# Performance work log

Hardware: AMD Instinct MI355X
Metric: run time of the kernel (lower is better)

## Reference

```python
import jax, jax.numpy as jnp
import numpy as np

INPUT_SIZE = 256
OUTPUT_SIZE = 128
N = 8192
SLOPE = 0.01
NEG_BIG = -9e15


def setup_inputs() -> dict:
    key = jax.random.key(0)
    k_h, k_adj, k_W, k_a = jax.random.split(key, 4)
    h = jax.random.normal(k_h, (N, INPUT_SIZE), dtype=jnp.float32)
    adj = jax.random.randint(k_adj, (N, N), 0, 2, dtype=jnp.int32)
    # xavier_uniform with gain=1.414
    gain = 1.414
    lim_W = gain * np.sqrt(6.0 / (INPUT_SIZE + OUTPUT_SIZE))
    W = jax.random.uniform(k_W, (INPUT_SIZE, OUTPUT_SIZE), dtype=jnp.float32, minval=-lim_W, maxval=lim_W)
    lim_a = gain * np.sqrt(6.0 / (2 * OUTPUT_SIZE + 1))
    a = jax.random.uniform(k_a, (2 * OUTPUT_SIZE, 1), dtype=jnp.float32, minval=-lim_a, maxval=lim_a)
    return {"h": h, "adj": adj, "W": W, "a": a}


def reference(h, adj, W, a):
    # Wh: [N, F]
    Wh = h @ W
    Fo = Wh.shape[1]
    # Original builds [N, N, 2F] concat then matmul with a; equivalent to
    # e[i, j] = leaky_relu(Wh[i] . a[:F] + Wh[j] . a[F:]) via broadcasting.
    src = Wh @ a[:Fo, 0]   # [N]
    dst = Wh @ a[Fo:, 0]   # [N]
    e = jax.nn.leaky_relu(src[:, None] + dst[None, :], negative_slope=SLOPE)  # [N, N]
    att = jnp.where(adj > 0, e, NEG_BIG)
    att = jax.nn.softmax(att, axis=1)
    return att @ Wh
```

## Files before the change

kernel.cpp:

```cpp
#include <hip/hip_runtime.h>
#include <hip/hip_bf16.h>

typedef unsigned short u16;
typedef unsigned char u8;
typedef unsigned int u32;
typedef __attribute__((ext_vector_type(8))) short short8;
typedef __attribute__((ext_vector_type(4))) float f32x4;

#define NN 8192
#define KIN 256
#define FOUT 128
#define KW 2048
#define L2E 1.4426950408889634f

__device__ __forceinline__ float exp2fast(float x) { return __builtin_amdgcn_exp2f(x); }

__device__ __forceinline__ u16 f2bf(float f) {
    u32 u = __float_as_uint(f);
    u32 r = ((u >> 16) & 1u) + 0x7fffu;
    return (u16)((u + r) >> 16);
}
__device__ __forceinline__ u32 pk_bf16(float a, float b) {
    union { __hip_bfloat162 h2; u32 u; } cv;
    cv.h2 = __float22bfloat162_rn(make_float2(a, b));
    return cv.u;
}
__device__ __forceinline__ u32 fkey(float f) {
    u32 b = __float_as_uint(f);
    return (b & 0x80000000u) ? ~b : (b | 0x80000000u);
}
__device__ __forceinline__ float funkey(u32 k) {
    u32 b = (k & 0x80000000u) ? (k & 0x7fffffffu) : ~k;
    return __uint_as_float(b);
}

__global__ __launch_bounds__(256) void k1_wh(
    const float* __restrict__ h, const float* __restrict__ W, const float* __restrict__ a,
    u16* __restrict__ whfrag,
    float* __restrict__ src, float* __restrict__ dl2e, u32* __restrict__ gmaxk)
{
    __shared__ float hT[64][36];
    __shared__ u16   lt[128][40];
    __shared__ float sd[32][2];
    const int t  = threadIdx.x;
    const int m0 = blockIdx.x * 32;
    const int rq = t >> 5, cq = t & 31;

    float acc[4][4];
#pragma unroll
    for (int i = 0; i < 4; i++)
#pragma unroll
        for (int j = 0; j < 4; j++) acc[i][j] = 0.f;
    if (t < 64) sd[t >> 1][t & 1] = 0.f;

    for (int kt = 0; kt < KIN; kt += 64) {
        __syncthreads();
#pragma unroll
        for (int s2 = 0; s2 < 2; s2++) {
            int f = s2 * 256 + t;
            int r = f >> 4, kc = (f & 15) * 4;
            float4 hv = *(const float4*)(h + (size_t)(m0 + r) * KIN + kt + kc);
            hT[kc + 0][r] = hv.x; hT[kc + 1][r] = hv.y;
            hT[kc + 2][r] = hv.z; hT[kc + 3][r] = hv.w;
        }
        __syncthreads();
        for (int k = 0; k < 64; k++) {
            float4 wv = *(const float4*)(W + (size_t)(kt + k) * FOUT + cq * 4);
            float h0 = hT[k][rq * 4 + 0], h1 = hT[k][rq * 4 + 1];
            float h2 = hT[k][rq * 4 + 2], h3 = hT[k][rq * 4 + 3];
            acc[0][0] += h0 * wv.x; acc[0][1] += h0 * wv.y; acc[0][2] += h0 * wv.z; acc[0][3] += h0 * wv.w;
            acc[1][0] += h1 * wv.x; acc[1][1] += h1 * wv.y; acc[1][2] += h1 * wv.z; acc[1][3] += h1 * wv.w;
            acc[2][0] += h2 * wv.x; acc[2][1] += h2 * wv.y; acc[2][2] += h2 * wv.z; acc[2][3] += h2 * wv.w;
            acc[3][0] += h3 * wv.x; acc[3][1] += h3 * wv.y; acc[3][2] += h3 * wv.z; acc[3][3] += h3 * wv.w;
        }
    }
#pragma unroll
    for (int i = 0; i < 4; i++) {
        float sp = 0.f, dp = 0.f;
#pragma unroll
        for (int j = 0; j < 4; j++) {
            sp += acc[i][j] * a[cq * 4 + j];
            dp += acc[i][j] * a[FOUT + cq * 4 + j];
            lt[cq * 4 + j][rq * 4 + i] = f2bf(acc[i][j]);
        }
        atomicAdd(&sd[rq * 4 + i][0], sp);
        atomicAdd(&sd[rq * 4 + i][1], dp);
    }
    __syncthreads();
    if (t < 32) { src[m0 + t] = sd[t][0]; dl2e[m0 + t] = sd[t][1] * L2E; }
    if (t < 64) {
        float v = (t < 32) ? sd[t][1] : -3.0e38f;
#pragma unroll
        for (int off = 32; off >= 1; off >>= 1) v = fmaxf(v, __shfl_down(v, off));
        if (t == 0) atomicMax(gmaxk, fkey(v));
    }
    const int kstep = blockIdx.x;
#pragma unroll
    for (int p = 0; p < 2; p++) {
        int f = p * 256 + t;
        int nt = f >> 6;
        int l  = f & 63;
        short8 v = *(const short8*)&lt[nt * 16 + (l & 15)][(l >> 4) * 8];
        *(short8*)(whfrag + ((size_t)(kstep * 8 + nt) * 64 + l) * 8) = v;
    }
}

__global__ __launch_bounds__(256, 4) void k2_attn(
    const int* __restrict__ adj, const float* __restrict__ src, const float* __restrict__ dl2e,
    const u16* __restrict__ whfrag, const u32* __restrict__ gmaxk,
    float* __restrict__ out)
{
    __shared__ u8  mask[4][16][512];
    __shared__ u16 Pall[4][16][40];
    const int t = threadIdx.x;
    const int lane = t & 63, wave = t >> 6;
    const int i0 = blockIdx.x * 16;
    const int l15 = lane & 15, quad = lane >> 4;
    const int r0 = lane >> 3, r1 = 8 + r0;
    const int co = (lane & 7) * 4;
    const int cbase = wave * KW;

#pragma unroll
    for (int r = 0; r < 16; r++) {
        const int* ap = adj + (size_t)(i0 + r) * NN + cbase;
#pragma unroll
        for (int c = 0; c < 8; c++) {
            int4 v = *(const int4*)(ap + c * 256 + lane * 4);
            mask[wave][r][c * 64 + lane] =
                (u8)((v.x > 0) | ((v.y > 0) << 1) | ((v.z > 0) << 2) | ((v.w > 0) << 3));
        }
    }

    const float gm = funkey(*gmaxk) * L2E;
    float s0 = src[i0 + r0] * L2E, s1 = src[i0 + r1] * L2E;
    float xm0 = s0 + gm, xm1 = s1 + gm;
    float C0 = fmaxf(xm0, 0.01f * xm0), C1 = fmaxf(xm1, 0.01f * xm1);
    const float y10 = s0 - C0, y20 = 0.01f * s0 - C0;
    const float y11 = s1 - C1, y21 = 0.01f * s1 - C1;

    u16 (*P)[40] = Pall[wave];
    f32x4 acc[8];
#pragma unroll
    for (int nt = 0; nt < 8; nt++) acc[nt] = {0.f, 0.f, 0.f, 0.f};
    float ps0 = 0.f, ps1 = 0.f;

    for (int kk = 0; kk < 64; ++kk) {
        const int kb = cbase + kk * 32;

        uint4 bv[8];
        const u16* wf = whfrag + ((size_t)((kb >> 5) * 8) * 64 + lane) * 8;
#pragma unroll
        for (int nt = 0; nt < 8; nt++)
            bv[nt] = *(const uint4*)(wf + (size_t)nt * 64 * 8);

        u32 n0 = mask[wave][r0][kk * 8 + (lane & 7)];
        u32 n1 = mask[wave][r1][kk * 8 + (lane & 7)];
        float4 d = *(const float4*)(dl2e + kb + co);
        {
            float x, p0, p1, p2, p3;
            x = fmaxf(y10 + d.x, y20 + 0.01f * d.x); p0 = exp2fast((n0 & 1u) ? x : -1.0e9f);
            x = fmaxf(y10 + d.y, y20 + 0.01f * d.y); p1 = exp2fast((n0 & 2u) ? x : -1.0e9f);
            x = fmaxf(y10 + d.z, y20 + 0.01f * d.z); p2 = exp2fast((n0 & 4u) ? x : -1.0e9f);
            x = fmaxf(y10 + d.w, y20 + 0.01f * d.w); p3 = exp2fast((n0 & 8u) ? x : -1.0e9f);
            ps0 += (p0 + p1) + (p2 + p3);
            *(uint2*)&P[r0][co] = make_uint2(pk_bf16(p0, p1), pk_bf16(p2, p3));
            x = fmaxf(y11 + d.x, y21 + 0.01f * d.x); p0 = exp2fast((n1 & 1u) ? x : -1.0e9f);
            x = fmaxf(y11 + d.y, y21 + 0.01f * d.y); p1 = exp2fast((n1 & 2u) ? x : -1.0e9f);
            x = fmaxf(y11 + d.z, y21 + 0.01f * d.z); p2 = exp2fast((n1 & 4u) ? x : -1.0e9f);
            x = fmaxf(y11 + d.w, y21 + 0.01f * d.w); p3 = exp2fast((n1 & 8u) ? x : -1.0e9f);
            ps1 += (p0 + p1) + (p2 + p3);
            *(uint2*)&P[r1][co] = make_uint2(pk_bf16(p0, p1), pk_bf16(p2, p3));
        }

        short8 af = *(const short8*)&P[l15][quad * 8];

#pragma unroll
        for (int nt = 0; nt < 8; nt++) {
            union { uint4 q; short8 s8; } bf; bf.q = bv[nt];
            acc[nt] = __builtin_amdgcn_mfma_f32_16x16x32_bf16(af, bf.s8, acc[nt], 0, 0, 0);
        }
    }

    ps0 += __shfl_down(ps0, 4, 8); ps0 += __shfl_down(ps0, 2, 8); ps0 += __shfl_down(ps0, 1, 8);
    ps1 += __shfl_down(ps1, 4, 8); ps1 += __shfl_down(ps1, 2, 8); ps1 += __shfl_down(ps1, 1, 8);
    float* pf = (float*)&Pall[wave][0][0];
    if ((lane & 7) == 0) { pf[r0] = ps0; pf[r1] = ps1; }

    float* ex = (float*)&mask[wave][0][0];
    {
        int crow = quad * 4, ccol = l15;
#pragma unroll
        for (int nt = 0; nt < 8; nt++)
#pragma unroll
            for (int reg = 0; reg < 4; reg++)
                ex[(crow + reg) * FOUT + nt * 16 + ccol] = acc[nt][reg];
    }
    __syncthreads();

    {
        int row = t >> 4, c8 = (t & 15) * 8;
        float s[8];
#pragma unroll
        for (int j = 0; j < 8; j++) s[j] = 0.f;
        float l = 0.f;
#pragma unroll
        for (int w = 0; w < 4; w++) {
            const float* exw = (const float*)&mask[w][0][0];
            const float* pfw = (const float*)&Pall[w][0][0];
            float4 v0 = *(const float4*)&exw[row * FOUT + c8];
            float4 v1 = *(const float4*)&exw[row * FOUT + c8 + 4];
            s[0] += v0.x; s[1] += v0.y; s[2] += v0.z; s[3] += v0.w;
            s[4] += v1.x; s[5] += v1.y; s[6] += v1.z; s[7] += v1.w;
            l += pfw[row];
        }
        float ri = 1.0f / l;
        float* op = out + (size_t)(i0 + row) * FOUT + c8;
        *(float4*)op       = make_float4(s[0] * ri, s[1] * ri, s[2] * ri, s[3] * ri);
        *(float4*)(op + 4) = make_float4(s[4] * ri, s[5] * ri, s[6] * ri, s[7] * ri);
    }
}

extern "C" void kernel_launch(void* const* d_in, const int* in_sizes, int n_in,
                              void* d_out, int out_size, void* d_ws, size_t ws_size,
                              hipStream_t stream) {
    const float* h   = (const float*)d_in[0];
    const int*   adj = (const int*)d_in[1];
    const float* W   = (const float*)d_in[2];
    const float* a   = (const float*)d_in[3];
    float* out = (float*)d_out;

    char* ws = (char*)d_ws;
    u16*   whfrag = (u16*)ws;
    float* src    = (float*)(ws + (2u << 20));
    float* dl2e   = src + NN;
    u32*   gmaxk  = (u32*)(dl2e + NN);

    (void)hipMemsetAsync(gmaxk, 0, sizeof(u32), stream);
    k1_wh<<<dim3(NN / 32), dim3(256), 0, stream>>>(h, W, a, whfrag, src, dl2e, gmaxk);
    k2_attn<<<dim3(NN / 16), dim3(256), 0, stream>>>(adj, src, dl2e, whfrag, gmaxk, out);
}
```

Measured before the change: 486.0 us.

## Split attention into probability-materialization pass and separate bf16 MFMA GEMM

Splits the fused attention kernel into two. The first is an elementwise kernel that reads adj, computes the exponentiated masked scores, writes them as bf16 in MFMA fragment layout to a 128MB workspace buffer, and accumulates row sums with atomics. The second is a plain GEMM that streams those fragments with a two-deep register prefetch against Wh. The goal is more parallelism and a simpler GEMM loop, paid for with an extra 128MB write plus read of the P matrix and per-row atomics.

Result: slower. 565.9 us (+16.4%).

```diff
diff --git a/kernel.cpp b/kernel.cpp
--- a/kernel.cpp
+++ b/kernel.cpp
@@ -10,7 +10,6 @@
 #define NN 8192
 #define KIN 256
 #define FOUT 128
-#define KW 2048
 #define L2E 1.4426950408889634f
 
 __device__ __forceinline__ float exp2fast(float x) { return __builtin_amdgcn_exp2f(x); }
@@ -105,115 +104,104 @@
     }
 }
 
-__global__ __launch_bounds__(256, 4) void k2_attn(
+__global__ __launch_bounds__(256) void k2a_p(
     const int* __restrict__ adj, const float* __restrict__ src, const float* __restrict__ dl2e,
-    const u16* __restrict__ whfrag, const u32* __restrict__ gmaxk,
-    float* __restrict__ out)
+    const u32* __restrict__ gmaxk, u16* __restrict__ pfrag, float* __restrict__ rsum)
 {
-    __shared__ u8  mask[4][16][512];
-    __shared__ u16 Pall[4][16][40];
+    const size_t idx = (size_t)blockIdx.x * 256 + threadIdx.x;
+    const int i = (int)(idx >> 11);
+    const int c = (int)(idx & 2047);
+
+    float s = src[i] * L2E;
+    float gm = funkey(*gmaxk) * L2E;
+    float xm = s + gm;
+    float C = fmaxf(xm, 0.01f * xm);
+    float y1 = s - C, y2 = 0.01f * s - C;
+
+    int4 av = *(const int4*)(adj + idx * 4);
+    float4 d = *(const float4*)(dl2e + c * 4);
+
+    float x, p0, p1, p2, p3;
+    x = fmaxf(y1 + d.x, y2 + 0.01f * d.x); p0 = exp2fast(av.x > 0 ? x : -1.0e9f);
+    x = fmaxf(y1 + d.y, y2 + 0.01f * d.y); p1 = exp2fast(av.y > 0 ? x : -1.0e9f);
+    x = fmaxf(y1 + d.z, y2 + 0.01f * d.z); p2 = exp2fast(av.z > 0 ? x : -1.0e9f);
+    x = fmaxf(y1 + d.w, y2 + 0.01f * d.w); p3 = exp2fast(av.w > 0 ? x : -1.0e9f);
+
+    {
+        int mt = i >> 4, ks = c >> 3;
+        int l = (i & 15) + ((c >> 1) & 3) * 16;
+        int e = (c & 1) * 4;
+        uint2 w = make_uint2(pk_bf16(p0, p1), pk_bf16(p2, p3));
+        *(uint2*)(pfrag + ((size_t)(mt * 256 + ks) * 512 + l * 8 + e)) = w;
+    }
+
+    float v = ((p0 + p1) + (p2 + p3));
+    v += __shfl_down(v, 32); v += __shfl_down(v, 16); v += __shfl_down(v, 8);
+    v += __shfl_down(v, 4);  v += __shfl_down(v, 2);  v += __shfl_down(v, 1);
+    if ((threadIdx.x & 63) == 0) atomicAdd(&rsum[i], v);
+}
+
+__global__ __launch_bounds__(256, 4) void k2c_gemm(
+    const u16* __restrict__ pfrag, const u16* __restrict__ whfrag,
+    const float* __restrict__ rsum, float* __restrict__ out)
+{
+    __shared__ float ex[4][16][FOUT];
     const int t = threadIdx.x;
     const int lane = t & 63, wave = t >> 6;
-    const int i0 = blockIdx.x * 16;
+    const int mt = blockIdx.x;
+    const int i0 = mt * 16;
     const int l15 = lane & 15, quad = lane >> 4;
-    const int r0 = lane >> 3, r1 = 8 + r0;
-    const int co = (lane & 7) * 4;
-    const int cbase = wave * KW;
-
-#pragma unroll
-    for (int r = 0; r < 16; r++) {
-        const int* ap = adj + (size_t)(i0 + r) * NN + cbase;
-#pragma unroll
-        for (int c = 0; c < 8; c++) {
-            int4 v = *(const int4*)(ap + c * 256 + lane * 4);
-            mask[wave][r][c * 64 + lane] =
-                (u8)((v.x > 0) | ((v.y > 0) << 1) | ((v.z > 0) << 2) | ((v.w > 0) << 3));
-        }
-    }
-
-    const float gm = funkey(*gmaxk) * L2E;
-    float s0 = src[i0 + r0] * L2E, s1 = src[i0 + r1] * L2E;
-    float xm0 = s0 + gm, xm1 = s1 + gm;
-    float C0 = fmaxf(xm0, 0.01f * xm0), C1 = fmaxf(xm1, 0.01f * xm1);
-    const float y10 = s0 - C0, y20 = 0.01f * s0 - C0;
-    const float y11 = s1 - C1, y21 = 0.01f * s1 - C1;
-
-    u16 (*P)[40] = Pall[wave];
+
     f32x4 acc[8];
 #pragma unroll
     for (int nt = 0; nt < 8; nt++) acc[nt] = {0.f, 0.f, 0.f, 0.f};
-    float ps0 = 0.f, ps1 = 0.f;
+
+    const u16* ap = pfrag + ((size_t)mt * 256 + wave * 64) * 512 + lane * 8;
+    uint4 a0 = *(const uint4*)ap;
+    uint4 a1 = *(const uint4*)(ap + 512);
 
     for (int kk = 0; kk < 64; ++kk) {
-        const int kb = cbase + kk * 32;
-
+        const int ks = wave * 64 + kk;
         uint4 bv[8];
-        const u16* wf = whfrag + ((size_t)((kb >> 5) * 8) * 64 + lane) * 8;
+        const u16* wf = whfrag + ((size_t)ks * 8 * 64 + lane) * 8;
 #pragma unroll
         for (int nt = 0; nt < 8; nt++)
             bv[nt] = *(const uint4*)(wf + (size_t)nt * 64 * 8);
 
-        u32 n0 = mask[wave][r0][kk * 8 + (lane & 7)];
-        u32 n1 = mask[wave][r1][kk * 8 + (lane & 7)];
-        float4 d = *(const float4*)(dl2e + kb + co);
-        {
-            float x, p0, p1, p2, p3;
-            x = fmaxf(y10 + d.x, y20 + 0.01f * d.x); p0 = exp2fast((n0 & 1u) ? x : -1.0e9f);
-            x = fmaxf(y10 + d.y, y20 + 0.01f * d.y); p1 = exp2fast((n0 & 2u) ? x : -1.0e9f);
-            x = fmaxf(y10 + d.z, y20 + 0.01f * d.z); p2 = exp2fast((n0 & 4u) ? x : -1.0e9f);
-            x = fmaxf(y10 + d.w, y20 + 0.01f * d.w); p3 = exp2fast((n0 & 8u) ? x : -1.0e9f);
-            ps0 += (p0 + p1) + (p2 + p3);
-            *(uint2*)&P[r0][co] = make_uint2(pk_bf16(p0, p1), pk_bf16(p2, p3));
-            x = fmaxf(y11 + d.x, y21 + 0.01f * d.x); p0 = exp2fast((n1 & 1u) ? x : -1.0e9f);
-            x = fmaxf(y11 + d.y, y21 + 0.01f * d.y); p1 = exp2fast((n1 & 2u) ? x : -1.0e9f);
-            x = fmaxf(y11 + d.z, y21 + 0.01f * d.z); p2 = exp2fast((n1 & 4u) ? x : -1.0e9f);
-            x = fmaxf(y11 + d.w, y21 + 0.01f * d.w); p3 = exp2fast((n1 & 8u) ? x : -1.0e9f);
-            ps1 += (p0 + p1) + (p2 + p3);
-            *(uint2*)&P[r1][co] = make_uint2(pk_bf16(p0, p1), pk_bf16(p2, p3));
-        }
-
-        short8 af = *(const short8*)&P[l15][quad * 8];
-
+        uint4 av = a0;
+        a0 = a1;
+        if (kk + 2 < 64) a1 = *(const uint4*)(ap + (size_t)(kk + 2) * 512);
+
+        union { uint4 q; short8 s8; } af; af.q = av;
 #pragma unroll
         for (int nt = 0; nt < 8; nt++) {
             union { uint4 q; short8 s8; } bf; bf.q = bv[nt];
-            acc[nt] = __builtin_amdgcn_mfma_f32_16x16x32_bf16(af, bf.s8, acc[nt], 0, 0, 0);
-        }
-    }
-
-    ps0 += __shfl_down(ps0, 4, 8); ps0 += __shfl_down(ps0, 2, 8); ps0 += __shfl_down(ps0, 1, 8);
-    ps1 += __shfl_down(ps1, 4, 8); ps1 += __shfl_down(ps1, 2, 8); ps1 += __shfl_down(ps1, 1, 8);
-    float* pf = (float*)&Pall[wave][0][0];
-    if ((lane & 7) == 0) { pf[r0] = ps0; pf[r1] = ps1; }
-
-    float* ex = (float*)&mask[wave][0][0];
+            acc[nt] = __builtin_amdgcn_mfma_f32_16x16x32_bf16(af.s8, bf.s8, acc[nt], 0, 0, 0);
+        }
+    }
+
     {
         int crow = quad * 4, ccol = l15;
 #pragma unroll
         for (int nt = 0; nt < 8; nt++)
 #pragma unroll
             for (int reg = 0; reg < 4; reg++)
-                ex[(crow + reg) * FOUT + nt * 16 + ccol] = acc[nt][reg];
+                ex[wave][crow + reg][nt * 16 + ccol] = acc[nt][reg];
     }
     __syncthreads();
-
     {
         int row = t >> 4, c8 = (t & 15) * 8;
         float s[8];
 #pragma unroll
         for (int j = 0; j < 8; j++) s[j] = 0.f;
-        float l = 0.f;
 #pragma unroll
         for (int w = 0; w < 4; w++) {
-            const float* exw = (const float*)&mask[w][0][0];
-            const float* pfw = (const float*)&Pall[w][0][0];
-            float4 v0 = *(const float4*)&exw[row * FOUT + c8];
-            float4 v1 = *(const float4*)&exw[row * FOUT + c8 + 4];
+            float4 v0 = *(const float4*)&ex[w][row][c8];
+            float4 v1 = *(const float4*)&ex[w][row][c8 + 4];
             s[0] += v0.x; s[1] += v0.y; s[2] += v0.z; s[3] += v0.w;
             s[4] += v1.x; s[5] += v1.y; s[6] += v1.z; s[7] += v1.w;
-            l += pfw[row];
-        }
-        float ri = 1.0f / l;
+        }
+        float ri = 1.0f / rsum[i0 + row];
         float* op = out + (size_t)(i0 + row) * FOUT + c8;
         *(float4*)op       = make_float4(s[0] * ri, s[1] * ri, s[2] * ri, s[3] * ri);
         *(float4*)(op + 4) = make_float4(s[4] * ri, s[5] * ri, s[6] * ri, s[7] * ri);
@@ -233,9 +221,13 @@
     u16*   whfrag = (u16*)ws;
     float* src    = (float*)(ws + (2u << 20));
     float* dl2e   = src + NN;
-    u32*   gmaxk  = (u32*)(dl2e + NN);
+    float* rsum   = dl2e + NN;
+    u32*   gmaxk  = (u32*)(rsum + NN);
+    u16*   pfrag  = (u16*)(ws + (16u << 20));
 
     (void)hipMemsetAsync(gmaxk, 0, sizeof(u32), stream);
+    (void)hipMemsetAsync(rsum, 0, NN * sizeof(float), stream);
     k1_wh<<<dim3(NN / 32), dim3(256), 0, stream>>>(h, W, a, whfrag, src, dl2e, gmaxk);
-    k2_attn<<<dim3(NN / 16), dim3(256), 0, stream>>>(adj, src, dl2e, whfrag, gmaxk, out);
-}
+    k2a_p<<<dim3((NN / 4) * (NN / 256)), dim3(256), 0, stream>>>(adj, src, dl2e, gmaxk, pfrag, rsum);
+    k2c_gemm<<<dim3(NN / 16), dim3(256), 0, stream>>>(pfrag, whfrag, rsum, out);
+}
```
